# Kernel tuning notes

Measured on AMD Instinct MI355X. Metric: run time of the kernel, lower is better.

## Reference

```python
import jax, jax.numpy as jnp
import numpy as np

N, E, G = 50000, 800000, 64
DIN, HID, OUT, ED = 128, 64, 96, 32
BN_EPS = 1e-5


def setup_inputs() -> dict:
    key = jax.random.key(0)
    ks = jax.random.split(key, 40)
    d = {}
    d["x"] = jax.random.normal(ks[0], (N, DIN), dtype=jnp.float32)
    d["edge_attr"] = jax.random.normal(ks[1], (E, ED), dtype=jnp.float32)
    d["edge_index"] = jax.random.randint(ks[2], (2, E), 0, N)
    d["batch"] = jnp.sort(jax.random.randint(ks[3], (N,), 0, G))
    dims = [(DIN, HID), (HID, HID), (HID, OUT)]  # (layer input dim, layer output dim)
    i = 4
    for l, (din, dout) in enumerate(dims):
        d[f"le{l}_w"] = jax.random.normal(ks[i], (ED, din), dtype=jnp.float32) * 0.05; i += 1
        d[f"le{l}_b"] = jnp.zeros((din,), dtype=jnp.float32)
        d[f"m{l}_w1"] = jax.random.normal(ks[i], (din, dout), dtype=jnp.float32) * 0.05; i += 1
        d[f"m{l}_b1"] = jnp.zeros((dout,), dtype=jnp.float32)
        d[f"m{l}_w2"] = jax.random.normal(ks[i], (dout, dout), dtype=jnp.float32) * 0.05; i += 1
        d[f"m{l}_b2"] = jnp.zeros((dout,), dtype=jnp.float32)
        d[f"bn{l}_g"] = jnp.ones((dout,), dtype=jnp.float32)
        d[f"bn{l}_b"] = jnp.zeros((dout,), dtype=jnp.float32)
        d[f"bn{l}_m"] = jax.random.normal(ks[i], (dout,), dtype=jnp.float32) * 0.01; i += 1
        d[f"bn{l}_v"] = jnp.ones((dout,), dtype=jnp.float32) + jax.random.uniform(ks[i], (dout,), dtype=jnp.float32) * 0.1; i += 1
    return d


def _gine_layer(x, src, dst, edge_attr, lew, leb, w1, b1, w2, b2,
                bng, bnb, bnm, bnv):
    # GINEConv: message = relu(x_j + Lin(edge_attr)); aggregate = sum into dst
    e = edge_attr @ lew + leb                      # [E, din]
    m = jax.nn.relu(x[src] + e)                    # [E, din]
    agg = jax.ops.segment_sum(m, dst, num_segments=x.shape[0])
    h = x + agg                                    # (1 + eps) * x + agg, eps = 0
    h = jax.nn.relu(h @ w1 + b1) @ w2 + b2         # 2-layer MLP
    # BatchNorm1d (eval: running stats) then ReLU; dropout is identity in eval
    h = (h - bnm) * (bng * jax.lax.rsqrt(bnv + BN_EPS)) + bnb
    return jax.nn.relu(h)


def reference(x, edge_attr,
              le0_w, le0_b, m0_w1, m0_b1, m0_w2, m0_b2, bn0_g, bn0_b, bn0_m, bn0_v,
              le1_w, le1_b, m1_w1, m1_b1, m1_w2, m1_b2, bn1_g, bn1_b, bn1_m, bn1_v,
              le2_w, le2_b, m2_w1, m2_b1, m2_w2, m2_b2, bn2_g, bn2_b, bn2_m, bn2_v,
              edge_index, batch):
    src, dst = edge_index[0], edge_index[1]
    h = _gine_layer(x, src, dst, edge_attr, le0_w, le0_b, m0_w1, m0_b1, m0_w2, m0_b2,
                    bn0_g, bn0_b, bn0_m, bn0_v)
    h = _gine_layer(h, src, dst, edge_attr, le1_w, le1_b, m1_w1, m1_b1, m1_w2, m1_b2,
                    bn1_g, bn1_b, bn1_m, bn1_v)
    h = _gine_layer(h, src, dst, edge_attr, le2_w, le2_b, m2_w1, m2_b1, m2_w2, m2_b2,
                    bn2_g, bn2_b, bn2_m, bn2_v)
    # global mean pool over graphs
    sums = jax.ops.segment_sum(h, batch, num_segments=G)            # [G, OUT]
    cnts = jax.ops.segment_sum(jnp.ones((h.shape[0],), h.dtype), batch, num_segments=G)
    return sums / jnp.maximum(cnts, 1.0)[:, None]
```

## Files before the change

### kernel.cpp

```cpp
#include <hip/hip_runtime.h>
#include <hip/hip_bf16.h>

#define N_NODES 50000
#define N_EDGES 800000
#define N_GRAPHS 64

__global__ __launch_bounds__(256) void hist_kernel(const int* __restrict__ ei,
                                                   int* __restrict__ deg, int E) {
  int e = blockIdx.x * 256 + threadIdx.x;
  if (e < E) atomicAdd(&deg[ei[E + e]], 1);
}

__global__ __launch_bounds__(1024) void scan_kernel(const int* __restrict__ deg,
                                                    int* __restrict__ row_start,
                                                    int* __restrict__ cursor, int N) {
  __shared__ int part[1024];
  const int t = threadIdx.x;
  const int C = (N + 1023) / 1024;
  const int b0 = min(t * C, N);
  const int b1 = min(b0 + C, N);
  int s = 0;
  for (int i = b0; i < b1; ++i) s += deg[i];
  part[t] = s;
  __syncthreads();
  for (int off = 1; off < 1024; off <<= 1) {
    int v = (t >= off) ? part[t - off] : 0;
    __syncthreads();
    part[t] += v;
    __syncthreads();
  }
  int ex = (t == 0) ? 0 : part[t - 1];
  for (int i = b0; i < b1; ++i) {
    row_start[i] = ex;
    cursor[i] = ex;
    ex += deg[i];
  }
  if (t == 1023) row_start[N] = part[1023];
}

__global__ __launch_bounds__(256) void scatter_kernel(const int* __restrict__ ei,
                                                      int* __restrict__ cursor,
                                                      int2* __restrict__ epair, int E) {
  int e = blockIdx.x * 256 + threadIdx.x;
  if (e < E) {
    int d = ei[E + e];
    int p = atomicAdd(&cursor[d], 1);
    epair[p] = make_int2(e, ei[e]);
  }
}

template <int DIN>
__global__ __launch_bounds__(256) void gine_gather(
    const float* __restrict__ x, const float* __restrict__ ea,
    const int* __restrict__ row_start, const int2* __restrict__ epair,
    const float* __restrict__ lew, const float* __restrict__ leb,
    float* __restrict__ hpre, int N) {
  constexpr int FPL = DIN / 64;
  const int lane = threadIdx.x & 63;
  const int wv = __builtin_amdgcn_readfirstlane(blockIdx.x * 4 + (threadIdx.x >> 6));
  const int nw = gridDim.x * 4;

  float w[32][FPL];
  float bb[FPL];
#pragma unroll
  for (int p = 0; p < FPL; ++p) bb[p] = leb[lane + 64 * p];
#pragma unroll
  for (int k = 0; k < 32; ++k)
#pragma unroll
    for (int p = 0; p < FPL; ++p) {
      w[k][p] = lew[k * DIN + lane + 64 * p];
      asm("" : "+v"(w[k][p]));
    }

  for (int n = wv; n < N; n += nw) {
    const int e0 = row_start[n];
    const int e1 = row_start[n + 1];
    float acc[FPL];
#pragma unroll
    for (int p = 0; p < FPL; ++p) acc[p] = 0.f;

    for (int i = e0; i < e1; ++i) {
      const int2 es = epair[i];
      const int e = __builtin_amdgcn_readfirstlane(es.x);
      const int s = __builtin_amdgcn_readfirstlane(es.y);
      const float* __restrict__ earow = ea + (size_t)e * 32;
      float t[FPL];
#pragma unroll
      for (int p = 0; p < FPL; ++p) t[p] = bb[p];
#pragma unroll
      for (int k = 0; k < 32; ++k) {
        const float eak = earow[k];
#pragma unroll
        for (int p = 0; p < FPL; ++p) t[p] = fmaf(eak, w[k][p], t[p]);
      }
#pragma unroll
      for (int p = 0; p < FPL; ++p) {
        const float m = t[p] + x[(size_t)s * DIN + lane + 64 * p];
        acc[p] += fmaxf(m, 0.f);
      }
    }
#pragma unroll
    for (int p = 0; p < FPL; ++p)
      hpre[(size_t)n * DIN + lane + 64 * p] =
          x[(size_t)n * DIN + lane + 64 * p] + acc[p];
  }
}

template <int K, int M, bool DO_BN>
__global__ void mlp_gemm(const float* __restrict__ in, const float* __restrict__ w,
                         const float* __restrict__ bias, const float* __restrict__ bng,
                         const float* __restrict__ bnb, const float* __restrict__ bnm,
                         const float* __restrict__ bnv, float* __restrict__ out, int N) {
  constexpr int Q = M / 4;
  constexpr int NPB = 8;
  __shared__ alignas(16) float ws_[K * M];
  __shared__ alignas(16) float hin[NPB * K];
  __shared__ alignas(16) float bnA[DO_BN ? M : 4];
  __shared__ alignas(16) float bnB[DO_BN ? M : 4];

  const int tid = threadIdx.x;
  const int bdim = Q * NPB;

  for (int i = tid; i < K * M / 4; i += bdim)
    ((float4*)ws_)[i] = ((const float4*)w)[i];
  if constexpr (DO_BN) {
    for (int f = tid; f < M; f += bdim) {
      float s = bng[f] * rsqrtf(bnv[f] + 1e-5f);
      bnA[f] = s;
      bnB[f] = bnb[f] - bnm[f] * s;
    }
  }
  const int nb = blockIdx.x * NPB;
  for (int i = tid; i < NPB * K; i += bdim) {
    const int dn = i / K;
    const int col = i - dn * K;
    const int n = nb + dn;
    hin[i] = (n < N) ? in[(size_t)n * K + col] : 0.f;
  }
  __syncthreads();

  const int ns = tid / Q;
  const int q = tid - ns * Q;
  const int n = nb + ns;

  float4 acc = ((const float4*)bias)[q];
#pragma unroll 8
  for (int k = 0; k < K; ++k) {
    const float hv = hin[ns * K + k];
    const float4 wv = ((const float4*)ws_)[k * Q + q];
    acc.x = fmaf(hv, wv.x, acc.x);
    acc.y = fmaf(hv, wv.y, acc.y);
    acc.z = fmaf(hv, wv.z, acc.z);
    acc.w = fmaf(hv, wv.w, acc.w);
  }
  if constexpr (DO_BN) {
    const float4 a = ((const float4*)bnA)[q];
    const float4 b = ((const float4*)bnB)[q];
    acc.x = fmaf(acc.x, a.x, b.x);
    acc.y = fmaf(acc.y, a.y, b.y);
    acc.z = fmaf(acc.z, a.z, b.z);
    acc.w = fmaf(acc.w, a.w, b.w);
  }
  acc.x = acc.x > 0.f ? acc.x : 0.f;
  acc.y = acc.y > 0.f ? acc.y : 0.f;
  acc.z = acc.z > 0.f ? acc.z : 0.f;
  acc.w = acc.w > 0.f ? acc.w : 0.f;
  if (n < N) ((float4*)out)[(size_t)n * Q + q] = acc;
}

__global__ __launch_bounds__(128) void pool_kernel(const float* __restrict__ h,
                                                   const int* __restrict__ batch,
                                                   float* __restrict__ sums,
                                                   int* __restrict__ cnt, int N) {
  const int f = threadIdx.x;
  const int chunk = (N + gridDim.x - 1) / gridDim.x;
  const int n0 = blockIdx.x * chunk;
  const int n1 = min(n0 + chunk, N);
  int curg = -1;
  float acc = 0.f;
  int c = 0;
  for (int n = n0; n < n1; ++n) {
    const int g = batch[n];
    if (g != curg) {
      if (curg >= 0) {
        if (f < 96) unsafeAtomicAdd(&sums[curg * 96 + f], acc);
        if (f == 0) atomicAdd(&cnt[curg], c);
      }
      curg = g;
      acc = 0.f;
      c = 0;
    }
    if (f < 96) acc += h[(size_t)n * 96 + f];
    ++c;
  }
  if (curg >= 0) {
    if (f < 96) unsafeAtomicAdd(&sums[curg * 96 + f], acc);
    if (f == 0) atomicAdd(&cnt[curg], c);
  }
}

__global__ void finalize_kernel(const float* __restrict__ sums,
                                const int* __restrict__ cnt, float* __restrict__ out) {
  const int i = blockIdx.x * blockDim.x + threadIdx.x;
  if (i < N_GRAPHS * 96) {
    const int g = i / 96;
    const float c = (float)cnt[g];
    out[i] = sums[i] / fmaxf(c, 1.f);
  }
}

extern "C" void kernel_launch(void* const* d_in, const int* in_sizes, int n_in,
                              void* d_out, int out_size, void* d_ws, size_t ws_size,
                              hipStream_t stream) {
  const int N = N_NODES;
  const int E = N_EDGES;

  const float* x = (const float*)d_in[0];
  const float* ea = (const float*)d_in[1];
  const int* ei = (const int*)d_in[2];
  const int* batch = (const int*)d_in[3];
  auto L = [&](int l, int idx) { return (const float*)d_in[4 + 10 * l + idx]; };

  int* iws = (int*)d_ws;
  int* deg = iws;
  int* row_start = deg + N;
  int* cursor = row_start + N + 1;
  int2* epair = (int2*)(iws + 150004);
  float* fws = (float*)(iws + 150004 + 2 * E);
  float* hpre = fws;
  float* t1 = hpre + (size_t)N * 128;
  float* hA = t1 + (size_t)N * 96;
  float* hB = hA + (size_t)N * 96;
  float* sums = hB + (size_t)N * 64;
  int* cnt = (int*)(sums + N_GRAPHS * 96);

  const int gE = (E + 255) / 256;
  const int gW = (N + 3) / 4;
  const int gN8 = (N + 7) / 8;

  hipMemsetAsync(deg, 0, (size_t)N * 4, stream);
  hist_kernel<<<gE, 256, 0, stream>>>(ei, deg, E);
  scan_kernel<<<1, 1024, 0, stream>>>(deg, row_start, cursor, N);
  scatter_kernel<<<gE, 256, 0, stream>>>(ei, cursor, epair, E);

  gine_gather<128><<<gW, 256, 0, stream>>>(x, ea, row_start, epair, L(0, 0), L(0, 1), hpre, N);
  mlp_gemm<128, 64, false><<<gN8, 128, 0, stream>>>(
      hpre, L(0, 2), L(0, 3), nullptr, nullptr, nullptr, nullptr, t1, N);
  mlp_gemm<64, 64, true><<<gN8, 128, 0, stream>>>(
      t1, L(0, 4), L(0, 5), L(0, 6), L(0, 7), L(0, 8), L(0, 9), hA, N);

  gine_gather<64><<<gW, 256, 0, stream>>>(hA, ea, row_start, epair, L(1, 0), L(1, 1), hpre, N);
  mlp_gemm<64, 64, false><<<gN8, 128, 0, stream>>>(
      hpre, L(1, 2), L(1, 3), nullptr, nullptr, nullptr, nullptr, t1, N);
  mlp_gemm<64, 64, true><<<gN8, 128, 0, stream>>>(
      t1, L(1, 4), L(1, 5), L(1, 6), L(1, 7), L(1, 8), L(1, 9), hB, N);

  gine_gather<64><<<gW, 256, 0, stream>>>(hB, ea, row_start, epair, L(2, 0), L(2, 1), hpre, N);
  mlp_gemm<64, 96, false><<<gN8, 192, 0, stream>>>(
      hpre, L(2, 2), L(2, 3), nullptr, nullptr, nullptr, nullptr, t1, N);
  mlp_gemm<96, 96, true><<<gN8, 192, 0, stream>>>(
      t1, L(2, 4), L(2, 5), L(2, 6), L(2, 7), L(2, 8), L(2, 9), hA, N);

  hipMemsetAsync(sums, 0, (size_t)(N_GRAPHS * 96 + N_GRAPHS) * 4, stream);
  pool_kernel<<<512, 128, 0, stream>>>(hA, batch, sums, cnt, N);
  finalize_kernel<<<48, 128, 0, stream>>>(sums, cnt, (float*)d_out);
}
```

Before: 978.3 us.

## Fuse two-layer MLP into one kernel and restructure edge gather per wave

Merges the two MLP GEMM kernels per layer into one kernel that holds the hidden activations in shared memory, and tiles 32 nodes per block with 4 rows per thread. This removes the intermediate global round trip and half the launches. The gather kernel now stages the edge-linear weights in LDS rather than registers, assigns one wave per 64-feature slice of a node instead of grid-striding, and processes 4 edges per iteration for more memory-level parallelism. In exchange, the gather reads weights from LDS on every edge and pays tail masking on partial edge groups.

Result: no change. 975.0 us (-0.3%).

```diff
diff --git a/kernel.cpp b/kernel.cpp
--- a/kernel.cpp
+++ b/kernel.cpp
@@ -55,117 +55,164 @@
     const int* __restrict__ row_start, const int2* __restrict__ epair,
     const float* __restrict__ lew, const float* __restrict__ leb,
     float* __restrict__ hpre, int N) {
-  constexpr int FPL = DIN / 64;
-  const int lane = threadIdx.x & 63;
-  const int wv = __builtin_amdgcn_readfirstlane(blockIdx.x * 4 + (threadIdx.x >> 6));
-  const int nw = gridDim.x * 4;
-
-  float w[32][FPL];
-  float bb[FPL];
-#pragma unroll
-  for (int p = 0; p < FPL; ++p) bb[p] = leb[lane + 64 * p];
-#pragma unroll
-  for (int k = 0; k < 32; ++k)
-#pragma unroll
-    for (int p = 0; p < FPL; ++p) {
-      w[k][p] = lew[k * DIN + lane + 64 * p];
-      asm("" : "+v"(w[k][p]));
-    }
-
-  for (int n = wv; n < N; n += nw) {
-    const int e0 = row_start[n];
-    const int e1 = row_start[n + 1];
-    float acc[FPL];
-#pragma unroll
-    for (int p = 0; p < FPL; ++p) acc[p] = 0.f;
-
-    for (int i = e0; i < e1; ++i) {
-      const int2 es = epair[i];
-      const int e = __builtin_amdgcn_readfirstlane(es.x);
-      const int s = __builtin_amdgcn_readfirstlane(es.y);
-      const float* __restrict__ earow = ea + (size_t)e * 32;
-      float t[FPL];
-#pragma unroll
-      for (int p = 0; p < FPL; ++p) t[p] = bb[p];
-#pragma unroll
-      for (int k = 0; k < 32; ++k) {
-        const float eak = earow[k];
-#pragma unroll
-        for (int p = 0; p < FPL; ++p) t[p] = fmaf(eak, w[k][p], t[p]);
+  constexpr int WPN = DIN / 64;
+  __shared__ float wlds[32 * DIN];
+  const int tid = threadIdx.x;
+  for (int i = tid; i < 32 * DIN / 4; i += 256)
+    ((float4*)wlds)[i] = ((const float4*)lew)[i];
+  __syncthreads();
+
+  const int gw = blockIdx.x * 4 + (tid >> 6);
+  if (gw >= N * WPN) return;
+  const int lane = tid & 63;
+  const int n = gw / WPN;
+  const int off = (gw % WPN) * 64 + lane;
+
+  const float bb = leb[off];
+  const int e0 = row_start[n];
+  const int e1 = row_start[n + 1];
+  float acc = 0.f;
+
+  for (int i = e0; i < e1; i += 4) {
+    int ee[4], ss[4];
+    float val[4];
+#pragma unroll
+    for (int j = 0; j < 4; ++j) {
+      const int idx = (i + j < e1) ? (i + j) : (e1 - 1);
+      const int2 p = epair[idx];
+      ee[j] = __builtin_amdgcn_readfirstlane(p.x);
+      ss[j] = __builtin_amdgcn_readfirstlane(p.y);
+      val[j] = (i + j < e1) ? 1.f : 0.f;
+    }
+    float xv[4], t[4];
+#pragma unroll
+    for (int j = 0; j < 4; ++j) {
+      xv[j] = x[(size_t)ss[j] * DIN + off];
+      t[j] = bb;
+    }
+    const float* __restrict__ r0 = ea + (size_t)ee[0] * 32;
+    const float* __restrict__ r1 = ea + (size_t)ee[1] * 32;
+    const float* __restrict__ r2 = ea + (size_t)ee[2] * 32;
+    const float* __restrict__ r3 = ea + (size_t)ee[3] * 32;
+#pragma unroll
+    for (int k = 0; k < 32; ++k) {
+      const float wk = wlds[k * DIN + off];
+      t[0] = fmaf(r0[k], wk, t[0]);
+      t[1] = fmaf(r1[k], wk, t[1]);
+      t[2] = fmaf(r2[k], wk, t[2]);
+      t[3] = fmaf(r3[k], wk, t[3]);
+    }
+#pragma unroll
+    for (int j = 0; j < 4; ++j) acc += val[j] * fmaxf(xv[j] + t[j], 0.f);
+  }
+  hpre[(size_t)n * DIN + off] = x[(size_t)n * DIN + off] + acc;
+}
+
+template <int K, int M>
+__global__ __launch_bounds__((M / 4) * 8) void mlp_fused(
+    const float* __restrict__ in, const float* __restrict__ w1,
+    const float* __restrict__ b1, const float* __restrict__ w2,
+    const float* __restrict__ b2, const float* __restrict__ bng,
+    const float* __restrict__ bnb, const float* __restrict__ bnm,
+    const float* __restrict__ bnv, float* __restrict__ out, int N) {
+  constexpr int NPB = 32;
+  constexpr int SK = K + 4;
+  constexpr int SH = M + 4;
+  constexpr int Q = M / 4;
+  constexpr int TH = Q * 8;
+  constexpr int R1 = K * M + NPB * SK;
+  constexpr int SZA = (R1 > M * M) ? R1 : (M * M);
+  __shared__ alignas(16) float smem[SZA + NPB * SH + 2 * M];
+  float* w1l = smem;
+  float* hin = smem + K * M;
+  float* w2l = smem;
+  float* h1 = smem + SZA;
+  float* bnA = h1 + NPB * SH;
+  float* bnB = bnA + M;
+
+  const int tid = threadIdx.x;
+  const int nb = blockIdx.x * NPB;
+
+  for (int i = tid; i < K * M / 4; i += TH)
+    ((float4*)w1l)[i] = ((const float4*)w1)[i];
+  for (int f = tid; f < M; f += TH) {
+    const float s = bng[f] * rsqrtf(bnv[f] + 1e-5f);
+    bnA[f] = s;
+    bnB[f] = bnb[f] - bnm[f] * s;
+  }
+  for (int i = tid; i < NPB * (K / 4); i += TH) {
+    const int dn = i / (K / 4);
+    const int kq = i % (K / 4);
+    const int n = nb + dn;
+    float4 v = make_float4(0.f, 0.f, 0.f, 0.f);
+    if (n < N) v = ((const float4*)(in + (size_t)n * K))[kq];
+    ((float4*)(hin + dn * SK))[kq] = v;
+  }
+  __syncthreads();
+
+  const int q = tid % Q;
+  const int ng = tid / Q;
+
+  {
+    const float4 bias = ((const float4*)b1)[q];
+    float4 a[4] = {bias, bias, bias, bias};
+#pragma unroll 4
+    for (int k = 0; k < K; ++k) {
+      const float4 wv = ((const float4*)w1l)[k * Q + q];
+#pragma unroll
+      for (int r = 0; r < 4; ++r) {
+        const float hv = hin[(ng * 4 + r) * SK + k];
+        a[r].x = fmaf(hv, wv.x, a[r].x);
+        a[r].y = fmaf(hv, wv.y, a[r].y);
+        a[r].z = fmaf(hv, wv.z, a[r].z);
+        a[r].w = fmaf(hv, wv.w, a[r].w);
       }
-#pragma unroll
-      for (int p = 0; p < FPL; ++p) {
-        const float m = t[p] + x[(size_t)s * DIN + lane + 64 * p];
-        acc[p] += fmaxf(m, 0.f);
+    }
+    __syncthreads();
+#pragma unroll
+    for (int r = 0; r < 4; ++r) {
+      float4 v = a[r];
+      v.x = fmaxf(v.x, 0.f);
+      v.y = fmaxf(v.y, 0.f);
+      v.z = fmaxf(v.z, 0.f);
+      v.w = fmaxf(v.w, 0.f);
+      ((float4*)(h1 + (ng * 4 + r) * SH))[q] = v;
+    }
+  }
+  for (int i = tid; i < M * M / 4; i += TH)
+    ((float4*)w2l)[i] = ((const float4*)w2)[i];
+  __syncthreads();
+
+  {
+    const float4 bias = ((const float4*)b2)[q];
+    float4 a[4] = {bias, bias, bias, bias};
+#pragma unroll 4
+    for (int k = 0; k < M; ++k) {
+      const float4 wv = ((const float4*)w2l)[k * Q + q];
+#pragma unroll
+      for (int r = 0; r < 4; ++r) {
+        const float hv = h1[(ng * 4 + r) * SH + k];
+        a[r].x = fmaf(hv, wv.x, a[r].x);
+        a[r].y = fmaf(hv, wv.y, a[r].y);
+        a[r].z = fmaf(hv, wv.z, a[r].z);
+        a[r].w = fmaf(hv, wv.w, a[r].w);
       }
     }
-#pragma unroll
-    for (int p = 0; p < FPL; ++p)
-      hpre[(size_t)n * DIN + lane + 64 * p] =
-          x[(size_t)n * DIN + lane + 64 * p] + acc[p];
-  }
-}
-
-template <int K, int M, bool DO_BN>
-__global__ void mlp_gemm(const float* __restrict__ in, const float* __restrict__ w,
-                         const float* __restrict__ bias, const float* __restrict__ bng,
-                         const float* __restrict__ bnb, const float* __restrict__ bnm,
-                         const float* __restrict__ bnv, float* __restrict__ out, int N) {
-  constexpr int Q = M / 4;
-  constexpr int NPB = 8;
-  __shared__ alignas(16) float ws_[K * M];
-  __shared__ alignas(16) float hin[NPB * K];
-  __shared__ alignas(16) float bnA[DO_BN ? M : 4];
-  __shared__ alignas(16) float bnB[DO_BN ? M : 4];
-
-  const int tid = threadIdx.x;
-  const int bdim = Q * NPB;
-
-  for (int i = tid; i < K * M / 4; i += bdim)
-    ((float4*)ws_)[i] = ((const float4*)w)[i];
-  if constexpr (DO_BN) {
-    for (int f = tid; f < M; f += bdim) {
-      float s = bng[f] * rsqrtf(bnv[f] + 1e-5f);
-      bnA[f] = s;
-      bnB[f] = bnb[f] - bnm[f] * s;
-    }
-  }
-  const int nb = blockIdx.x * NPB;
-  for (int i = tid; i < NPB * K; i += bdim) {
-    const int dn = i / K;
-    const int col = i - dn * K;
-    const int n = nb + dn;
-    hin[i] = (n < N) ? in[(size_t)n * K + col] : 0.f;
-  }
-  __syncthreads();
-
-  const int ns = tid / Q;
-  const int q = tid - ns * Q;
-  const int n = nb + ns;
-
-  float4 acc = ((const float4*)bias)[q];
-#pragma unroll 8
-  for (int k = 0; k < K; ++k) {
-    const float hv = hin[ns * K + k];
-    const float4 wv = ((const float4*)ws_)[k * Q + q];
-    acc.x = fmaf(hv, wv.x, acc.x);
-    acc.y = fmaf(hv, wv.y, acc.y);
-    acc.z = fmaf(hv, wv.z, acc.z);
-    acc.w = fmaf(hv, wv.w, acc.w);
-  }
-  if constexpr (DO_BN) {
-    const float4 a = ((const float4*)bnA)[q];
-    const float4 b = ((const float4*)bnB)[q];
-    acc.x = fmaf(acc.x, a.x, b.x);
-    acc.y = fmaf(acc.y, a.y, b.y);
-    acc.z = fmaf(acc.z, a.z, b.z);
-    acc.w = fmaf(acc.w, a.w, b.w);
-  }
-  acc.x = acc.x > 0.f ? acc.x : 0.f;
-  acc.y = acc.y > 0.f ? acc.y : 0.f;
-  acc.z = acc.z > 0.f ? acc.z : 0.f;
-  acc.w = acc.w > 0.f ? acc.w : 0.f;
-  if (n < N) ((float4*)out)[(size_t)n * Q + q] = acc;
+    const float4 A = ((const float4*)bnA)[q];
+    const float4 B = ((const float4*)bnB)[q];
+#pragma unroll
+    for (int r = 0; r < 4; ++r) {
+      const int n = nb + ng * 4 + r;
+      if (n < N) {
+        float4 v = a[r];
+        v.x = fmaxf(fmaf(v.x, A.x, B.x), 0.f);
+        v.y = fmaxf(fmaf(v.y, A.y, B.y), 0.f);
+        v.z = fmaxf(fmaf(v.z, A.z, B.z), 0.f);
+        v.w = fmaxf(fmaf(v.w, A.w, B.w), 0.f);
+        ((float4*)(out + (size_t)n * M))[q] = v;
+      }
+    }
+  }
 }
 
 __global__ __launch_bounds__(128) void pool_kernel(const float* __restrict__ h,
@@ -228,38 +275,33 @@
   int2* epair = (int2*)(iws + 150004);
   float* fws = (float*)(iws + 150004 + 2 * E);
   float* hpre = fws;
-  float* t1 = hpre + (size_t)N * 128;
-  float* hA = t1 + (size_t)N * 96;
+  float* hA = hpre + (size_t)N * 128;
   float* hB = hA + (size_t)N * 96;
   float* sums = hB + (size_t)N * 64;
   int* cnt = (int*)(sums + N_GRAPHS * 96);
 
   const int gE = (E + 255) / 256;
-  const int gW = (N + 3) / 4;
-  const int gN8 = (N + 7) / 8;
+  const int gN32 = (N + 31) / 32;
 
   hipMemsetAsync(deg, 0, (size_t)N * 4, stream);
   hist_kernel<<<gE, 256, 0, stream>>>(ei, deg, E);
   scan_kernel<<<1, 1024, 0, stream>>>(deg, row_start, cursor, N);
   scatter_kernel<<<gE, 256, 0, stream>>>(ei, cursor, epair, E);
 
-  gine_gather<128><<<gW, 256, 0, stream>>>(x, ea, row_start, epair, L(0, 0), L(0, 1), hpre, N);
-  mlp_gemm<128, 64, false><<<gN8, 128, 0, stream>>>(
-      hpre, L(0, 2), L(0, 3), nullptr, nullptr, nullptr, nullptr, t1, N);
-  mlp_gemm<64, 64, true><<<gN8, 128, 0, stream>>>(
-      t1, L(0, 4), L(0, 5), L(0, 6), L(0, 7), L(0, 8), L(0, 9), hA, N);
-
-  gine_gather<64><<<gW, 256, 0, stream>>>(hA, ea, row_start, epair, L(1, 0), L(1, 1), hpre, N);
-  mlp_gemm<64, 64, false><<<gN8, 128, 0, stream>>>(
-      hpre, L(1, 2), L(1, 3), nullptr, nullptr, nullptr, nullptr, t1, N);
-  mlp_gemm<64, 64, true><<<gN8, 128, 0, stream>>>(
-      t1, L(1, 4), L(1, 5), L(1, 6), L(1, 7), L(1, 8), L(1, 9), hB, N);
-
-  gine_gather<64><<<gW, 256, 0, stream>>>(hB, ea, row_start, epair, L(2, 0), L(2, 1), hpre, N);
-  mlp_gemm<64, 96, false><<<gN8, 192, 0, stream>>>(
-      hpre, L(2, 2), L(2, 3), nullptr, nullptr, nullptr, nullptr, t1, N);
-  mlp_gemm<96, 96, true><<<gN8, 192, 0, stream>>>(
-      t1, L(2, 4), L(2, 5), L(2, 6), L(2, 7), L(2, 8), L(2, 9), hA, N);
+  gine_gather<128><<<(N * 2 + 3) / 4, 256, 0, stream>>>(
+      x, ea, row_start, epair, L(0, 0), L(0, 1), hpre, N);
+  mlp_fused<128, 64><<<gN32, 128, 0, stream>>>(
+      hpre, L(0, 2), L(0, 3), L(0, 4), L(0, 5), L(0, 6), L(0, 7), L(0, 8), L(0, 9), hA, N);
+
+  gine_gather<64><<<(N + 3) / 4, 256, 0, stream>>>(
+      hA, ea, row_start, epair, L(1, 0), L(1, 1), hpre, N);
+  mlp_fused<64, 64><<<gN32, 128, 0, stream>>>(
+      hpre, L(1, 2), L(1, 3), L(1, 4), L(1, 5), L(1, 6), L(1, 7), L(1, 8), L(1, 9), hB, N);
+
+  gine_gather<64><<<(N + 3) / 4, 256, 0, stream>>>(
+      hB, ea, row_start, epair, L(2, 0), L(2, 1), hpre, N);
+  mlp_fused<64, 96><<<gN32, 192, 0, stream>>>(
+      hpre, L(2, 2), L(2, 3), L(2, 4), L(2, 5), L(2, 6), L(2, 7), L(2, 8), L(2, 9), hA, N);
 
   hipMemsetAsync(sums, 0, (size_t)(N_GRAPHS * 96 + N_GRAPHS) * 4, stream);
   pool_kernel<<<512, 128, 0, stream>>>(hA, batch, sums, cnt, N);
```
